# Kernel optimization log

Measured on AMD Instinct MI355X. Metric: run time of the kernel, lower is better.

The kernel has to match this reference:

```python
import jax, jax.numpy as jnp
import numpy as np

BN_EPS = 1e-5
NORM_EPS = 1e-12  # F.normalize default eps


def reference(x, conv_w, bn_gamma, bn_beta):
    # 1x1 conv dimension reduction: [B,2048,H,W] -> [B,256,H,W]
    z = jnp.einsum('bchw,dc->bdhw', x, conv_w)
    # BatchNorm2d (training-mode batch statistics) + ReLU
    mu = z.mean(axis=(0, 2, 3), keepdims=True)
    var = z.var(axis=(0, 2, 3), keepdims=True)
    z = (z - mu) / jnp.sqrt(var + BN_EPS)
    z = z * bn_gamma.reshape(1, -1, 1, 1) + bn_beta.reshape(1, -1, 1, 1)
    z = jax.nn.relu(z)

    B, d, h, w = z.shape
    M = h * w
    xm = z.reshape(B, d, M)
    # Covpool: y = x I_hat x^T with I_hat = (I - 11^T/M)/M == centered 2nd moment
    xc = xm - xm.mean(axis=-1, keepdims=True)
    cov = jnp.einsum('bdm,bem->bde', xc, xc) / M  # [B,d,d]

    # Eigen decomposition (cov is symmetric PSD; SVD of PSD == eigh)
    s, U = jnp.linalg.eigh(cov)  # s: [B,d], U: [B,d,d]
    eps = jnp.finfo(cov.dtype).eps
    s = jnp.maximum(s, eps)

    # ExponentialInverse: U exp(-S) U^T
    inv_x = jnp.einsum('bid,bd,bjd->bij', U, jnp.exp(-s), U)
    # Power (matrix sqrt): U S^{1/2} U^T
    out = jnp.einsum('bid,bd,bjd->bij', U, jnp.sqrt(s), U)

    # attention = out @ inv_x^T  (inv_x is symmetric, transpose kept for fidelity)
    att = jnp.einsum('bij,bkj->bik', out, inv_x)
    flat = att.reshape(B, -1)
    nrm = jnp.maximum(jnp.linalg.norm(flat, axis=1, keepdims=True), NORM_EPS)
    normalized = (flat / nrm).reshape(att.shape)
    att = out * (att / normalized)

    y = att + out
    iu = jnp.triu_indices(d)
    return y[:, iu[0], iu[1]]  # [B, d*(d+1)/2]


def setup_inputs() -> dict:
    key = jax.random.key(0)
    k1, k2 = jax.random.split(key)
    x = jax.random.normal(k1, (32, 2048, 28, 28), dtype=jnp.float32)
    # kaiming-normal fan_out scaling for 1x1 conv: std = sqrt(2/fan_out)=sqrt(2/256)
    conv_w = jax.random.normal(k2, (256, 2048), dtype=jnp.float32) * np.sqrt(2.0 / 256.0)
    bn_gamma = jnp.ones((256,), dtype=jnp.float32)
    bn_beta = jnp.zeros((256,), dtype=jnp.float32)
    return {'x': x, 'conv_w': conv_w, 'bn_gamma': bn_gamma, 'bn_beta': bn_beta}
```

## Files before the change

### kernel.cpp

```cpp
#include <hip/hip_runtime.h>


typedef unsigned short u16;
typedef __attribute__((ext_vector_type(8))) short bf16x8;
typedef __attribute__((ext_vector_type(4))) float f32x4;

__device__ __forceinline__ u16 f2bf(float f) {
  unsigned u = __builtin_bit_cast(unsigned, f);
  u += 0x7FFFu + ((u >> 16) & 1u);
  return (u16)(u >> 16);
}
__device__ __forceinline__ float bf2f(u16 h) {
  unsigned u = ((unsigned)h) << 16;
  return __builtin_bit_cast(float, u);
}

__device__ __forceinline__
void mm_core(const u16* __restrict__ Ah, const u16* __restrict__ Al,
             const u16* __restrict__ Bh, const u16* __restrict__ Bl,
             long boff, int row0, int col0,
             u16 (*lds)[128][8][8], f32x4 acc[4][4])
{
  const int tid = threadIdx.x;
  const int wave = tid >> 6, lane = tid & 63;
  const int wm = wave >> 1, wn = wave & 1;
  const int mL = lane & 15, q = lane >> 4;
  const u16* baseA[2] = {Ah + boff, Al + boff};
  const u16* baseB[2] = {Bh + boff, Bl + boff};

  for (int k0 = 0; k0 < 256; k0 += 64) {
    __syncthreads();
#pragma unroll
    for (int it = 0; it < 16; ++it) {
      const int t = it >> 2;
      const int r = ((it & 3) << 8) + tid;
      const int m = r >> 3, c = r & 7;
      const u16* src = (t < 2 ? baseA[t] : baseB[t - 2])
                     + (long)((t < 2 ? row0 : col0) + m) * 256 + k0 + c * 8;
      const uint4 v = *reinterpret_cast<const uint4*>(src);
      *reinterpret_cast<uint4*>(&lds[t][m][c ^ (m & 7)][0]) = v;
    }
    __syncthreads();
#pragma unroll
    for (int kk = 0; kk < 2; ++kk) {
      bf16x8 ah[4], al[4], bh[4], bl[4];
#pragma unroll
      for (int i = 0; i < 4; ++i) {
        const int ma = wm * 64 + i * 16 + mL;
        const int ca = (kk * 4 + q) ^ (ma & 7);
        ah[i] = *reinterpret_cast<const bf16x8*>(&lds[0][ma][ca][0]);
        al[i] = *reinterpret_cast<const bf16x8*>(&lds[1][ma][ca][0]);
        const int nb = wn * 64 + i * 16 + mL;
        const int cb = (kk * 4 + q) ^ (nb & 7);
        bh[i] = *reinterpret_cast<const bf16x8*>(&lds[2][nb][cb][0]);
        bl[i] = *reinterpret_cast<const bf16x8*>(&lds[3][nb][cb][0]);
      }
#pragma unroll
      for (int i = 0; i < 4; ++i)
#pragma unroll
        for (int j = 0; j < 4; ++j) {
          acc[i][j] = __builtin_amdgcn_mfma_f32_16x16x32_bf16(ah[i], bh[j], acc[i][j], 0, 0, 0);
          acc[i][j] = __builtin_amdgcn_mfma_f32_16x16x32_bf16(ah[i], bl[j], acc[i][j], 0, 0, 0);
          acc[i][j] = __builtin_amdgcn_mfma_f32_16x16x32_bf16(al[i], bh[j], acc[i][j], 0, 0, 0);
        }
    }
  }
}

template<int MB>
__global__ __launch_bounds__(256)
void fuse_k(const u16* __restrict__ A0, const u16* __restrict__ B0, u16* __restrict__ C0,
            float al0, float b10, float dg0, const float* __restrict__ cf0,
            const u16* __restrict__ A1, const u16* __restrict__ B1, u16* __restrict__ C1,
            u16* __restrict__ D1, float al1, float b11, float dg1,
            float hc1, float hc2, float hc3, const float* __restrict__ cf1, long LO)
{
  __shared__ u16 lds[4][128][8][8];
  int z = blockIdx.z;
  const bool hB = (z >= 32);
  const u16 *Ah, *Bh; u16 *C, *D = nullptr;
  float al, b1, dg; const float* cf;
  if (!hB) { Ah = A0; Bh = B0; C = C0; al = al0; b1 = b10; dg = dg0; cf = cf0; }
  else { z -= 32; Ah = A1; Bh = B1; C = C1; D = D1; al = al1; b1 = b11; dg = dg1; cf = cf1; }
  const long boff = (long)z * 65536;
  const int row0 = blockIdx.y * 128, col0 = blockIdx.x * 128;
  const int wave = threadIdx.x >> 6, lane = threadIdx.x & 63;
  const int wm = wave >> 1, wn = wave & 1;
  const int mL = lane & 15, q = lane >> 4;

  f32x4 acc[4][4];
#pragma unroll
  for (int i = 0; i < 4; ++i)
#pragma unroll
    for (int j = 0; j < 4; ++j) acc[i][j] = {0.f, 0.f, 0.f, 0.f};

  mm_core(Ah, Ah + LO, Bh, Bh + LO, boff, row0, col0, lds, acc);

#pragma unroll
  for (int i = 0; i < 4; ++i) {
    const int rbase = row0 + wm * 64 + i * 16 + q * 4;
#pragma unroll
    for (int j = 0; j < 4; ++j) {
      const int cc = col0 + wn * 64 + j * 16 + mL;
#pragma unroll
      for (int rg = 0; rg < 4; ++rg) {
        const int rr = rbase + rg;
        const long o = boff + (long)rr * 256 + cc;
        const float vr = acc[i][j][rg];
        if (MB == 1 && hB) {
          u16 h = f2bf(vr);
          C[o] = h; C[o + LO] = f2bf(vr - bf2f(h));
          float hv = fmaf(vr, hc1, cf[o] * hc2);
          if (rr == cc) hv += hc3;
          h = f2bf(hv);
          D[o] = h; D[o + LO] = f2bf(hv - bf2f(h));
        } else {
          float v = al * vr;
          if (cf) v = fmaf(b1, cf[o], v);
          if (rr == cc) v += dg;
          const u16 h = f2bf(v);
          C[o] = h; C[o + LO] = f2bf(v - bf2f(h));
        }
      }
    }
  }
}

__global__ __launch_bounds__(256)
void gemm2_pair_k(const u16* __restrict__ A0, const u16* __restrict__ B0, u16* __restrict__ C0,
                  const u16* __restrict__ A1, const u16* __restrict__ B1, u16* __restrict__ C1,
                  long LO)
{
  __shared__ u16 lds[4][128][8][8];
  int z = blockIdx.z;
  const u16 *Ah, *Bh; u16* Chp;
  if (z < 32) { Ah = A0; Bh = B0; Chp = C0; }
  else { z -= 32; Ah = A1; Bh = B1; Chp = C1; }
  const long boff = (long)z * 65536;
  const int row0 = blockIdx.y * 128, col0 = blockIdx.x * 128;
  const int wave = threadIdx.x >> 6, lane = threadIdx.x & 63;
  const int wm = wave >> 1, wn = wave & 1;
  const int mL = lane & 15, q = lane >> 4;

  f32x4 acc[4][4];
#pragma unroll
  for (int i = 0; i < 4; ++i)
#pragma unroll
    for (int j = 0; j < 4; ++j) acc[i][j] = {0.f, 0.f, 0.f, 0.f};

  mm_core(Ah, Ah + LO, Bh, Bh + LO, boff, row0, col0, lds, acc);

#pragma unroll
  for (int i = 0; i < 4; ++i) {
    const int rbase = row0 + wm * 64 + i * 16 + q * 4;
#pragma unroll
    for (int j = 0; j < 4; ++j) {
      const int cc = col0 + wn * 64 + j * 16 + mL;
#pragma unroll
      for (int rg = 0; rg < 4; ++rg) {
        const long o = boff + (long)(rbase + rg) * 256 + cc;
        const float v = acc[i][j][rg];
        const u16 h = f2bf(v);
        Chp[o] = h; Chp[o + LO] = f2bf(v - bf2f(h));
      }
    }
  }
}

template<int MODE>
__global__ __launch_bounds__(256)
void gemmN64_k(const u16* __restrict__ Ah, const u16* __restrict__ Al,
               const u16* __restrict__ Bh, const u16* __restrict__ Bl,
               u16* __restrict__ Ch, u16* __restrict__ Cl,
               const float* __restrict__ cf, float alpha, float b1, float diag,
               float* __restrict__ attn2)
{
  __shared__ u16 ldsA[2][128][8][8];
  __shared__ u16 ldsB[2][64][8][8];
  const long boff = (long)blockIdx.z * 65536;
  const int row0 = blockIdx.y * 128, col0 = blockIdx.x * 64;
  const int tid = threadIdx.x;
  const int wave = tid >> 6, lane = tid & 63;
  const int wm = wave >> 1, wn = wave & 1;
  const int mL = lane & 15, q = lane >> 4;
  const u16* baseA[2] = {Ah + boff, Al + boff};
  const u16* baseB[2] = {Bh + boff, Bl + boff};

  f32x4 acc[4][2];
#pragma unroll
  for (int i = 0; i < 4; ++i)
#pragma unroll
    for (int j = 0; j < 2; ++j) acc[i][j] = {0.f, 0.f, 0.f, 0.f};

  for (int k0 = 0; k0 < 256; k0 += 64) {
    __syncthreads();
#pragma unroll
    for (int it = 0; it < 8; ++it) {
      const int t = it >> 2;
      const int r = ((it & 3) << 8) + tid;
      const int m = r >> 3, c = r & 7;
      const uint4 v = *reinterpret_cast<const uint4*>(
          baseA[t] + (long)(row0 + m) * 256 + k0 + c * 8);
      *reinterpret_cast<uint4*>(&ldsA[t][m][c ^ (m & 7)][0]) = v;
    }
#pragma unroll
    for (int it = 0; it < 4; ++it) {
      const int t = it >> 1;
      const int r = ((it & 1) << 8) + tid;
      const int m = r >> 3, c = r & 7;
      const uint4 v = *reinterpret_cast<const uint4*>(
          baseB[t] + (long)(col0 + m) * 256 + k0 + c * 8);
      *reinterpret_cast<uint4*>(&ldsB[t][m][c ^ (m & 7)][0]) = v;
    }
    __syncthreads();
#pragma unroll
    for (int kk = 0; kk < 2; ++kk) {
      bf16x8 ah[4], alo[4], bh[2], bl[2];
#pragma unroll
      for (int i = 0; i < 4; ++i) {
        const int ma = wm * 64 + i * 16 + mL;
        const int ca = (kk * 4 + q) ^ (ma & 7);
        ah[i]  = *reinterpret_cast<const bf16x8*>(&ldsA[0][ma][ca][0]);
        alo[i] = *reinterpret_cast<const bf16x8*>(&ldsA[1][ma][ca][0]);
      }
#pragma unroll
      for (int j = 0; j < 2; ++j) {
        const int nb = wn * 32 + j * 16 + mL;
        const int cb = (kk * 4 + q) ^ (nb & 7);
        bh[j] = *reinterpret_cast<const bf16x8*>(&ldsB[0][nb][cb][0]);
        bl[j] = *reinterpret_cast<const bf16x8*>(&ldsB[1][nb][cb][0]);
      }
#pragma unroll
      for (int i = 0; i < 4; ++i)
#pragma unroll
        for (int j = 0; j < 2; ++j) {
          acc[i][j] = __builtin_amdgcn_mfma_f32_16x16x32_bf16(ah[i],  bh[j], acc[i][j], 0, 0, 0);
          acc[i][j] = __builtin_amdgcn_mfma_f32_16x16x32_bf16(ah[i],  bl[j], acc[i][j], 0, 0, 0);
          acc[i][j] = __builtin_amdgcn_mfma_f32_16x16x32_bf16(alo[i], bh[j], acc[i][j], 0, 0, 0);
        }
    }
  }

  if (MODE == 2) {
    float ssum = 0.f;
#pragma unroll
    for (int i = 0; i < 4; ++i)
#pragma unroll
      for (int j = 0; j < 2; ++j)
#pragma unroll
        for (int rg = 0; rg < 4; ++rg) ssum = fmaf(acc[i][j][rg], acc[i][j][rg], ssum);
#pragma unroll
    for (int o = 32; o > 0; o >>= 1) ssum += __shfl_down(ssum, o);
    __syncthreads();
    float* red = (float*)&ldsA[0][0][0][0];
    if (lane == 0) red[wave] = ssum;
    __syncthreads();
    if (tid == 0)
      atomicAdd(attn2 + blockIdx.z, red[0] + red[1] + red[2] + red[3]);
    return;
  }

#pragma unroll
  for (int i = 0; i < 4; ++i) {
    const int rbase = row0 + wm * 64 + i * 16 + q * 4;
#pragma unroll
    for (int j = 0; j < 2; ++j) {
      const int cc = col0 + wn * 32 + j * 16 + mL;
#pragma unroll
      for (int rg = 0; rg < 4; ++rg) {
        const int rr = rbase + rg;
        const long o = boff + (long)rr * 256 + cc;
        float v = alpha * acc[i][j][rg];
        if (cf) v = fmaf(b1, cf[o], v);
        if (rr == cc) v += diag;
        const u16 h = f2bf(v);
        Ch[o] = h; Cl[o] = f2bf(v - bf2f(h));
      }
    }
  }
}

__global__ __launch_bounds__(256)
void conv_k(const u16* __restrict__ wb, const float* __restrict__ x,
            float* __restrict__ z)
{
  __shared__ u16 ldsA[128][8][8];
  __shared__ u16 ldsB[128][8][8];
  const int tid = threadIdx.x;
  const int b = blockIdx.z;
  const int n0 = blockIdx.x * 128;
  const int m0 = blockIdx.y * 128;
  const int wave = tid >> 6, lane = tid & 63;
  const int wm = wave >> 1, wn = wave & 1;
  const int mL = lane & 15, q = lane >> 4;
  const float* xb = x + (long)b * 2048 * 784;

  f32x4 acc[4][4];
#pragma unroll
  for (int i = 0; i < 4; ++i)
#pragma unroll
    for (int j = 0; j < 4; ++j) acc[i][j] = {0.f, 0.f, 0.f, 0.f};

  for (int k0 = 0; k0 < 2048; k0 += 64) {
    __syncthreads();
#pragma unroll
    for (int it = 0; it < 4; ++it) {
      const int g = it * 256 + tid;
      const int m = g >> 3, c = g & 7;
      const uint4 v = *reinterpret_cast<const uint4*>(
          wb + (long)(m0 + m) * 2048 + k0 + c * 8);
      *reinterpret_cast<uint4*>(&ldsA[m][c ^ (m & 7)][0]) = v;
    }
    {
      const int kg = tid >> 5, nc = tid & 31;
      const int nbase = nc * 4;
      const int gn = n0 + nbase;
#pragma unroll
      for (int half = 0; half < 2; ++half) {
        const int kbase = kg * 4 + half * 32;
        float vv[4][4];
#pragma unroll
        for (int jk = 0; jk < 4; ++jk) {
          const int gk = k0 + kbase + jk;
          float4 f = make_float4(0.f, 0.f, 0.f, 0.f);
          if (gn < 784) f = *reinterpret_cast<const float4*>(xb + (long)gk * 784 + gn);
          vv[jk][0] = f.x; vv[jk][1] = f.y; vv[jk][2] = f.z; vv[jk][3] = f.w;
        }
        const int c = kbase >> 3, ko = kbase & 7;
#pragma unroll
        for (int jn = 0; jn < 4; ++jn) {
          const int n = nbase + jn;
          ushort4 u;
          u.x = f2bf(vv[0][jn]); u.y = f2bf(vv[1][jn]);
          u.z = f2bf(vv[2][jn]); u.w = f2bf(vv[3][jn]);
          *reinterpret_cast<ushort4*>(&ldsB[n][c ^ (n & 7)][ko]) = u;
        }
      }
    }
    __syncthreads();
#pragma unroll
    for (int kk = 0; kk < 2; ++kk) {
      bf16x8 af[4], bfv[4];
#pragma unroll
      for (int i = 0; i < 4; ++i) {
        const int ma = wm * 64 + i * 16 + mL;
        af[i] = *reinterpret_cast<const bf16x8*>(&ldsA[ma][(kk * 4 + q) ^ (ma & 7)][0]);
        const int nb = wn * 64 + i * 16 + mL;
        bfv[i] = *reinterpret_cast<const bf16x8*>(&ldsB[nb][(kk * 4 + q) ^ (nb & 7)][0]);
      }
#pragma unroll
      for (int i = 0; i < 4; ++i)
#pragma unroll
        for (int j = 0; j < 4; ++j)
          acc[i][j] = __builtin_amdgcn_mfma_f32_16x16x32_bf16(af[i], bfv[j], acc[i][j], 0, 0, 0);
    }
  }
#pragma unroll
  for (int i = 0; i < 4; ++i) {
    const int rbase = m0 + wm * 64 + i * 16 + q * 4;
#pragma unroll
    for (int j = 0; j < 4; ++j) {
      const int cc = n0 + wn * 64 + j * 16 + mL;
      if (cc >= 784) continue;
#pragma unroll
      for (int rg = 0; rg < 4; ++rg)
        z[((long)b * 256 + rbase + rg) * 784 + cc] = acc[i][j][rg];
    }
  }
}

__global__ __launch_bounds__(256)
void gram_k(const u16* __restrict__ zb, const float* __restrict__ rs,
            float* __restrict__ cov, u16* __restrict__ C2h, u16* __restrict__ C2l)
{
  __shared__ u16 lds[2][128][8][8];
  const int tid = threadIdx.x;
  const int b = blockIdx.z;
  const int col0 = blockIdx.x * 128, row0 = blockIdx.y * 128;
  const int wave = tid >> 6, lane = tid & 63;
  const int wm = wave >> 1, wn = wave & 1;
  const int mL = lane & 15, q = lane >> 4;
  const u16* zbb = zb + (long)b * 256 * 832;

  f32x4 acc[4][4];
#pragma unroll
  for (int i = 0; i < 4; ++i)
#pragma unroll
    for (int j = 0; j < 4; ++j) acc[i][j] = {0.f, 0.f, 0.f, 0.f};

  for (int k0 = 0; k0 < 832; k0 += 64) {
    __syncthreads();
#pragma unroll
    for (int it = 0; it < 8; ++it) {
      const int t = it >> 2;
      const int r = ((it & 3) << 8) + tid;
      const int m = r >> 3, c = r & 7;
      const int grow = (t == 0 ? row0 : col0) + m;
      const uint4 v = *reinterpret_cast<const uint4*>(zbb + (long)grow * 832 + k0 + c * 8);
      *reinterpret_cast<uint4*>(&lds[t][m][c ^ (m & 7)][0]) = v;
    }
    __syncthreads();
#pragma unroll
    for (int kk = 0; kk < 2; ++kk) {
      bf16x8 af[4], bfv[4];
#pragma unroll
      for (int i = 0; i < 4; ++i) {
        const int ma = wm * 64 + i * 16 + mL;
        af[i] = *reinterpret_cast<const bf16x8*>(&lds[0][ma][(kk * 4 + q) ^ (ma & 7)][0]);
        const int nb = wn * 64 + i * 16 + mL;
        bfv[i] = *reinterpret_cast<const bf16x8*>(&lds[1][nb][(kk * 4 + q) ^ (nb & 7)][0]);
      }
#pragma unroll
      for (int i = 0; i < 4; ++i)
#pragma unroll
        for (int j = 0; j < 4; ++j)
          acc[i][j] = __builtin_amdgcn_mfma_f32_16x16x32_bf16(af[i], bfv[j], acc[i][j], 0, 0, 0);
    }
  }
  const float inv_m = 1.f / 784.f;
#pragma unroll
  for (int i = 0; i < 4; ++i) {
    const int rr0 = row0 + wm * 64 + i * 16 + q * 4;
#pragma unroll
    for (int j = 0; j < 4; ++j) {
      const int cc = col0 + wn * 64 + j * 16 + mL;
      const float mu_c = rs[b * 256 + cc] * inv_m;
#pragma unroll
      for (int rg = 0; rg < 4; ++rg) {
        const int rr = rr0 + rg;
        const float mu_r = rs[b * 256 + rr] * inv_m;
        const long o = ((long)b * 256 + rr) * 256 + cc;
        const float cv = fmaf(acc[i][j][rg], inv_m, -mu_r * mu_c);
        cov[o] = cv;
        const u16 h = f2bf(cv);
        C2h[o] = h; C2l[o] = f2bf(cv - bf2f(h));
      }
    }
  }
}

__global__ __launch_bounds__(256)
void bn_stats_k(const float* __restrict__ z, float* __restrict__ ps,
                float* __restrict__ pq)
{
  const int d = blockIdx.x, sl = blockIdx.y, t = threadIdx.x;
  const int lane = t & 63, wid = t >> 6;
  __shared__ float ws[4], wq[4];
  float s = 0.f, qq = 0.f;
  for (int b = sl * 4; b < sl * 4 + 4; ++b) {
    const float* p = z + ((long)b * 256 + d) * 784;
    for (int m = t; m < 784; m += 256) {
      const float v = p[m];
      s += v; qq = fmaf(v, v, qq);
    }
  }
#pragma unroll
  for (int o = 32; o > 0; o >>= 1) { s += __shfl_down(s, o); qq += __shfl_down(qq, o); }
  if (lane == 0) { ws[wid] = s; wq[wid] = qq; }
  __syncthreads();
  if (t == 0) {
    ps[d * 8 + sl] = ws[0] + ws[1] + ws[2] + ws[3];
    pq[d * 8 + sl] = wq[0] + wq[1] + wq[2] + wq[3];
  }
}

__global__ __launch_bounds__(256)
void bn_apply_k(const float* __restrict__ z, const float* __restrict__ gamma,
                const float* __restrict__ beta, const float* __restrict__ ps,
                const float* __restrict__ pq, u16* __restrict__ zb,
                float* __restrict__ rs)
{
  const int d = blockIdx.x, b = blockIdx.y, t = threadIdx.x;
  const int lane = t & 63, wid = t >> 6;
  __shared__ float bc[2], ws[4];
  if (t == 0) {
    float sum = 0.f, sq = 0.f;
#pragma unroll
    for (int s8 = 0; s8 < 8; ++s8) { sum += ps[d * 8 + s8]; sq += pq[d * 8 + s8]; }
    const float inv_n = 1.f / 25088.f;
    const float mean = sum * inv_n;
    const float var = sq * inv_n - mean * mean;
    const float sc = gamma[d] * rsqrtf(var + 1e-5f);
    bc[0] = sc; bc[1] = fmaf(-mean, sc, beta[d]);
  }
  __syncthreads();
  const float sc = bc[0], sh = bc[1];
  const float* p = z + ((long)b * 256 + d) * 784;
  u16* qp = zb + ((long)b * 256 + d) * 832;
  float rsum = 0.f;
  for (int m = t; m < 832; m += 256) {
    const float v = (m < 784) ? fmaxf(fmaf(p[m], sc, sh), 0.f) : 0.f;
    qp[m] = f2bf(v);
    rsum += v;
  }
#pragma unroll
  for (int o = 32; o > 0; o >>= 1) rsum += __shfl_down(rsum, o);
  if (lane == 0) ws[wid] = rsum;
  __syncthreads();
  if (t == 0) rs[b * 256 + d] = ws[0] + ws[1] + ws[2] + ws[3];
}

__global__ __launch_bounds__(1024)
void power_k(const float* __restrict__ cov, float* __restrict__ s,
             float* __restrict__ attn2)
{
  const int b = blockIdx.x, tid = threadIdx.x;
  const int i = tid & 255, g = tid >> 8;
  const float* A = cov + (long)b * 65536;
  __shared__ float v[256];
  __shared__ float part[4][256];
  __shared__ float red[4];
  if (g == 0) v[i] = 1.f;
  __syncthreads();
  float lam = 1.f;
  for (int it = 0; it < 10; ++it) {
    float u = 0.f;
    const int jb = g * 64;
#pragma unroll 8
    for (int j = jb; j < jb + 64; ++j) u = fmaf(A[(long)j * 256 + i], v[j], u);
    part[g][i] = u;
    __syncthreads();
    if (g == 0) {
      u = part[0][i] + part[1][i] + part[2][i] + part[3][i];
      float ss = u * u;
#pragma unroll
      for (int o = 32; o > 0; o >>= 1) ss += __shfl_down(ss, o);
      if ((i & 63) == 0) red[i >> 6] = ss;
    }
    __syncthreads();
    lam = sqrtf(red[0] + red[1] + red[2] + red[3]);
    if (g == 0) v[i] = u / lam;
    __syncthreads();
  }
  if (tid == 0) { s[b] = 1.8f / lam; attn2[b] = 0.f; }
}

__global__ __launch_bounds__(256)
void init_k(const float* __restrict__ cov, const float* __restrict__ s,
            u16* __restrict__ Yh, u16* __restrict__ Yl,
            u16* __restrict__ Th, u16* __restrict__ Tl)
{
  const int b = blockIdx.y, i = blockIdx.x, j = threadIdx.x;
  const long o = ((long)b * 256 + i) * 256 + j;
  const float a = cov[o] * s[b];
  u16 h = f2bf(a);
  Yh[o] = h; Yl[o] = f2bf(a - bf2f(h));
  float tv = -0.5f * a;
  if (i == j) tv += 1.5f;
  h = f2bf(tv);
  Th[o] = h; Tl[o] = f2bf(tv - bf2f(h));
}

__global__ __launch_bounds__(256)
void out_k(const u16* __restrict__ Yh, const u16* __restrict__ Yl,
           const float* __restrict__ s, const float* __restrict__ attn2,
           float* __restrict__ out)
{
  const int i = blockIdx.x, b = blockIdx.y, j = threadIdx.x;
  if (j < i) return;
  const float inv = rsqrtf(s[b]);
  const float nrm = fmaxf(sqrtf(fmaxf(attn2[b], 0.f)) * inv, 1e-12f);
  const float scv = inv * (1.f + nrm);
  const long o = ((long)b * 256 + i) * 256 + j;
  const long off = (long)b * 32896 + (long)i * 256 - (long)i * (i - 1) / 2 + (j - i);
  out[off] = (bf2f(Yh[o]) + bf2f(Yl[o])) * scv;
}

__global__ __launch_bounds__(256)
void cast_w_k(const float* __restrict__ w, u16* __restrict__ wb)
{
  const int idx = blockIdx.x * 256 + threadIdx.x;
  wb[idx] = f2bf(w[idx]);
}

extern "C" void kernel_launch(void* const* d_in, const int* in_sizes, int n_in,
                              void* d_out, int out_size, void* d_ws, size_t ws_size,
                              hipStream_t stream)
{
  const float* x     = (const float*)d_in[0];
  const float* w     = (const float*)d_in[1];
  const float* gamma = (const float*)d_in[2];
  const float* beta  = (const float*)d_in[3];
  float* out = (float*)d_out;

  const long PS = 4194304;
  const long LO = 2097152;
  u16* S[9];
  for (int k = 0; k < 9; ++k) S[k] = (u16*)d_ws + (long)k * PS;
  char* base = (char*)d_ws;
  float* z   = (float*)(base + 75497472);
  u16*   zb  = (u16*)(base + 101187584);
  float* cov = (float*)(base + 114819072);
  u16*   wbuf = (u16*)(base + 114819072);
  float* st  = (float*)(base + 123207680);
  float* sv = st, *attn2 = st + 32, *rs = st + 64;
  float* ps = st + 64 + 8192, *pq = ps + 2048;
  u16 *C2 = S[5], *V = S[6], *Ha = S[7], *Hb = S[8];

  const dim3 blk(256);
  const dim3 gP(2, 2, 64);
  const dim3 gT(4, 2, 32);
  const dim3 gE(256, 32);

  cast_w_k<<<dim3(2048), blk, 0, stream>>>(w, wbuf);
  conv_k<<<dim3(7, 2, 32), blk, 0, stream>>>(wbuf, x, z);
  bn_stats_k<<<dim3(256, 8), blk, 0, stream>>>(z, ps, pq);
  bn_apply_k<<<dim3(256, 32), blk, 0, stream>>>(z, gamma, beta, ps, pq, zb, rs);
  gram_k<<<dim3(2, 2, 32), blk, 0, stream>>>(zb, rs, cov, C2, C2 + LO);
  power_k<<<dim3(32), dim3(1024), 0, stream>>>(cov, sv, attn2);
  init_k<<<gE, blk, 0, stream>>>(cov, sv, S[0], S[0] + LO, S[1], S[1] + LO);

  fuse_k<1><<<gP, blk, 0, stream>>>(
      S[0], S[1], S[2], 1.f, 0.f, 0.f, (const float*)nullptr,
      C2, C2, V, Ha, 1.f, 0.f, 0.f,
      1.f / 40320.f, -1.f / 5040.f, 1.f / 720.f, cov, LO);

  int iY = 2, iZ = 1, fa = 0, fb = 3, fc = 4;
  for (int it = 1; it <= 7; ++it) {
    const int iT = fa;
    if (it == 1)
      fuse_k<0><<<gP, blk, 0, stream>>>(
          S[iZ], S[iY], S[iT], -0.5f, 0.f, 1.5f, (const float*)nullptr,
          V, Ha, Hb, (u16*)nullptr, 1.f, -1.f / 120.f, 1.f / 24.f,
          0.f, 0.f, 0.f, cov, LO);
    else if (it == 2)
      fuse_k<0><<<gP, blk, 0, stream>>>(
          S[iZ], S[iY], S[iT], -0.5f, 0.f, 1.5f, (const float*)nullptr,
          V, Hb, Ha, (u16*)nullptr, 1.f, -1.f / 6.f, 0.5f,
          0.f, 0.f, 0.f, cov, LO);
    else if (it == 3)
      fuse_k<0><<<gP, blk, 0, stream>>>(
          S[iZ], S[iY], S[iT], -0.5f, 0.f, 1.5f, (const float*)nullptr,
          V, Ha, Hb, (u16*)nullptr, 1.f, -1.f, 1.f,
          0.f, 0.f, 0.f, cov, LO);
    else
      gemmN64_k<0><<<gT, blk, 0, stream>>>(
          S[iZ], S[iZ] + LO, S[iY], S[iY] + LO, S[iT], S[iT] + LO,
          (const float*)nullptr, -0.5f, 0.f, 1.5f, (float*)nullptr);
    if (it < 7) {
      gemm2_pair_k<<<gP, blk, 0, stream>>>(S[iY], S[iT], S[fb],
                                           S[iT], S[iZ], S[fc], LO);
      const int nY = fb, nZ = fc;
      fa = iY; fb = iZ; fc = iT;
      iY = nY; iZ = nZ;
    } else {
      gemmN64_k<0><<<gT, blk, 0, stream>>>(
          S[iY], S[iY] + LO, S[iT], S[iT] + LO, S[fb], S[fb] + LO,
          (const float*)nullptr, 1.f, 0.f, 0.f, (float*)nullptr);
      iY = fb;
    }
  }

  gemmN64_k<2><<<gT, blk, 0, stream>>>(
      S[iY], S[iY] + LO, Hb, Hb + LO, (u16*)nullptr, (u16*)nullptr,
      (const float*)nullptr, 1.f, 0.f, 0.f, attn2);
  out_k<<<gE, blk, 0, stream>>>(S[iY], S[iY] + LO, sv, attn2, out);
}
```

Before: 739.0 us.

## Split conv GEMM along K with smaller M tiles and sum partials in BN

The 1x1 conv GEMM is split into two K halves with 64-row M tiles, quadrupling the block count to fill the GPU better. The two partial outputs go to separate buffers and are summed inside the BN statistics and apply kernels. The cost is that x is re-read by more M tiles, and an extra fp32 z buffer is written and read twice. The x load path is also reorganized into 8 consecutive k rows per thread with two LDS stores.

```diff
diff --git a/kernel.cpp b/kernel.cpp
--- a/kernel.cpp
+++ b/kernel.cpp
@@ -282,89 +282,96 @@
 
 __global__ __launch_bounds__(256)
 void conv_k(const u16* __restrict__ wb, const float* __restrict__ x,
-            float* __restrict__ z)
-{
-  __shared__ u16 ldsA[128][8][8];
+            float* __restrict__ z0, float* __restrict__ z1)
+{
+  __shared__ u16 ldsA[64][8][8];
   __shared__ u16 ldsB[128][8][8];
   const int tid = threadIdx.x;
   const int b = blockIdx.z;
   const int n0 = blockIdx.x * 128;
-  const int m0 = blockIdx.y * 128;
+  const int m0 = (blockIdx.y & 3) * 64;
+  const int ks = blockIdx.y >> 2;
+  const int kb0 = ks * 1024;
   const int wave = tid >> 6, lane = tid & 63;
   const int wm = wave >> 1, wn = wave & 1;
   const int mL = lane & 15, q = lane >> 4;
   const float* xb = x + (long)b * 2048 * 784;
-
-  f32x4 acc[4][4];
-#pragma unroll
-  for (int i = 0; i < 4; ++i)
+  float* zp = (ks == 0 ? z0 : z1);
+
+  f32x4 acc[2][4];
+#pragma unroll
+  for (int i = 0; i < 2; ++i)
 #pragma unroll
     for (int j = 0; j < 4; ++j) acc[i][j] = {0.f, 0.f, 0.f, 0.f};
 
-  for (int k0 = 0; k0 < 2048; k0 += 64) {
-    __syncthreads();
-#pragma unroll
-    for (int it = 0; it < 4; ++it) {
+  const int kc = tid >> 5, nc = tid & 31;
+  const int nbase = nc * 4;
+  const int gn = n0 + nbase;
+
+  for (int k0 = 0; k0 < 1024; k0 += 64) {
+    const int kg = kb0 + k0;
+    __syncthreads();
+#pragma unroll
+    for (int it = 0; it < 2; ++it) {
       const int g = it * 256 + tid;
       const int m = g >> 3, c = g & 7;
       const uint4 v = *reinterpret_cast<const uint4*>(
-          wb + (long)(m0 + m) * 2048 + k0 + c * 8);
+          wb + (long)(m0 + m) * 2048 + kg + c * 8);
       *reinterpret_cast<uint4*>(&ldsA[m][c ^ (m & 7)][0]) = v;
     }
     {
-      const int kg = tid >> 5, nc = tid & 31;
-      const int nbase = nc * 4;
-      const int gn = n0 + nbase;
-#pragma unroll
-      for (int half = 0; half < 2; ++half) {
-        const int kbase = kg * 4 + half * 32;
-        float vv[4][4];
-#pragma unroll
-        for (int jk = 0; jk < 4; ++jk) {
-          const int gk = k0 + kbase + jk;
-          float4 f = make_float4(0.f, 0.f, 0.f, 0.f);
-          if (gn < 784) f = *reinterpret_cast<const float4*>(xb + (long)gk * 784 + gn);
-          vv[jk][0] = f.x; vv[jk][1] = f.y; vv[jk][2] = f.z; vv[jk][3] = f.w;
-        }
-        const int c = kbase >> 3, ko = kbase & 7;
-#pragma unroll
-        for (int jn = 0; jn < 4; ++jn) {
-          const int n = nbase + jn;
-          ushort4 u;
-          u.x = f2bf(vv[0][jn]); u.y = f2bf(vv[1][jn]);
-          u.z = f2bf(vv[2][jn]); u.w = f2bf(vv[3][jn]);
-          *reinterpret_cast<ushort4*>(&ldsB[n][c ^ (n & 7)][ko]) = u;
-        }
+      float vv[8][4];
+#pragma unroll
+      for (int jk = 0; jk < 8; ++jk) {
+        float4 f = make_float4(0.f, 0.f, 0.f, 0.f);
+        if (gn < 784)
+          f = *reinterpret_cast<const float4*>(xb + (long)(kg + kc * 8 + jk) * 784 + gn);
+        vv[jk][0] = f.x; vv[jk][1] = f.y; vv[jk][2] = f.z; vv[jk][3] = f.w;
+      }
+#pragma unroll
+      for (int jn = 0; jn < 4; ++jn) {
+        const int n = nbase + jn;
+        const int ch = kc ^ (n & 7);
+        ushort4 ua, ub;
+        ua.x = f2bf(vv[0][jn]); ua.y = f2bf(vv[1][jn]);
+        ua.z = f2bf(vv[2][jn]); ua.w = f2bf(vv[3][jn]);
+        ub.x = f2bf(vv[4][jn]); ub.y = f2bf(vv[5][jn]);
+        ub.z = f2bf(vv[6][jn]); ub.w = f2bf(vv[7][jn]);
+        *reinterpret_cast<ushort4*>(&ldsB[n][ch][0]) = ua;
+        *reinterpret_cast<ushort4*>(&ldsB[n][ch][4]) = ub;
       }
     }
     __syncthreads();
 #pragma unroll
     for (int kk = 0; kk < 2; ++kk) {
-      bf16x8 af[4], bfv[4];
-#pragma unroll
-      for (int i = 0; i < 4; ++i) {
-        const int ma = wm * 64 + i * 16 + mL;
+      bf16x8 af[2], bfv[4];
+#pragma unroll
+      for (int i = 0; i < 2; ++i) {
+        const int ma = wm * 32 + i * 16 + mL;
         af[i] = *reinterpret_cast<const bf16x8*>(&ldsA[ma][(kk * 4 + q) ^ (ma & 7)][0]);
-        const int nb = wn * 64 + i * 16 + mL;
-        bfv[i] = *reinterpret_cast<const bf16x8*>(&ldsB[nb][(kk * 4 + q) ^ (nb & 7)][0]);
-      }
-#pragma unroll
-      for (int i = 0; i < 4; ++i)
+      }
+#pragma unroll
+      for (int j = 0; j < 4; ++j) {
+        const int nb = wn * 64 + j * 16 + mL;
+        bfv[j] = *reinterpret_cast<const bf16x8*>(&ldsB[nb][(kk * 4 + q) ^ (nb & 7)][0]);
+      }
+#pragma unroll
+      for (int i = 0; i < 2; ++i)
 #pragma unroll
         for (int j = 0; j < 4; ++j)
           acc[i][j] = __builtin_amdgcn_mfma_f32_16x16x32_bf16(af[i], bfv[j], acc[i][j], 0, 0, 0);
     }
   }
 #pragma unroll
-  for (int i = 0; i < 4; ++i) {
-    const int rbase = m0 + wm * 64 + i * 16 + q * 4;
+  for (int i = 0; i < 2; ++i) {
+    const int rbase = m0 + wm * 32 + i * 16 + q * 4;
 #pragma unroll
     for (int j = 0; j < 4; ++j) {
       const int cc = n0 + wn * 64 + j * 16 + mL;
       if (cc >= 784) continue;
 #pragma unroll
       for (int rg = 0; rg < 4; ++rg)
-        z[((long)b * 256 + rbase + rg) * 784 + cc] = acc[i][j][rg];
+        zp[((long)b * 256 + rbase + rg) * 784 + cc] = acc[i][j][rg];
     }
   }
 }
@@ -440,17 +447,17 @@
 }
 
 __global__ __launch_bounds__(256)
-void bn_stats_k(const float* __restrict__ z, float* __restrict__ ps,
-                float* __restrict__ pq)
+void bn_stats_k(const float* __restrict__ z0, const float* __restrict__ z1,
+                float* __restrict__ ps, float* __restrict__ pq)
 {
   const int d = blockIdx.x, sl = blockIdx.y, t = threadIdx.x;
   const int lane = t & 63, wid = t >> 6;
   __shared__ float ws[4], wq[4];
   float s = 0.f, qq = 0.f;
   for (int b = sl * 4; b < sl * 4 + 4; ++b) {
-    const float* p = z + ((long)b * 256 + d) * 784;
+    const long off = ((long)b * 256 + d) * 784;
     for (int m = t; m < 784; m += 256) {
-      const float v = p[m];
+      const float v = z0[off + m] + z1[off + m];
       s += v; qq = fmaf(v, v, qq);
     }
   }
@@ -465,10 +472,10 @@
 }
 
 __global__ __launch_bounds__(256)
-void bn_apply_k(const float* __restrict__ z, const float* __restrict__ gamma,
-                const float* __restrict__ beta, const float* __restrict__ ps,
-                const float* __restrict__ pq, u16* __restrict__ zb,
-                float* __restrict__ rs)
+void bn_apply_k(const float* __restrict__ z0, const float* __restrict__ z1,
+                const float* __restrict__ gamma, const float* __restrict__ beta,
+                const float* __restrict__ ps, const float* __restrict__ pq,
+                u16* __restrict__ zb, float* __restrict__ rs)
 {
   const int d = blockIdx.x, b = blockIdx.y, t = threadIdx.x;
   const int lane = t & 63, wid = t >> 6;
@@ -485,11 +492,12 @@
   }
   __syncthreads();
   const float sc = bc[0], sh = bc[1];
-  const float* p = z + ((long)b * 256 + d) * 784;
+  const long off = ((long)b * 256 + d) * 784;
   u16* qp = zb + ((long)b * 256 + d) * 832;
   float rsum = 0.f;
   for (int m = t; m < 832; m += 256) {
-    const float v = (m < 784) ? fmaxf(fmaf(p[m], sc, sh), 0.f) : 0.f;
+    const float v = (m < 784)
+        ? fmaxf(fmaf(z0[off + m] + z1[off + m], sc, sh), 0.f) : 0.f;
     qp[m] = f2bf(v);
     rsum += v;
   }
@@ -588,11 +596,12 @@
   u16* S[9];
   for (int k = 0; k < 9; ++k) S[k] = (u16*)d_ws + (long)k * PS;
   char* base = (char*)d_ws;
-  float* z   = (float*)(base + 75497472);
-  u16*   zb  = (u16*)(base + 101187584);
-  float* cov = (float*)(base + 114819072);
-  u16*   wbuf = (u16*)(base + 114819072);
-  float* st  = (float*)(base + 123207680);
+  float* z0  = (float*)(base + 75497472);
+  float* z1  = (float*)(base + 101187584);
+  u16*   zb  = (u16*)(base + 126877696);
+  float* cov = (float*)(base + 140509184);
+  u16*   wbuf = (u16*)(base + 140509184);
+  float* st  = (float*)(base + 148897792);
   float* sv = st, *attn2 = st + 32, *rs = st + 64;
   float* ps = st + 64 + 8192, *pq = ps + 2048;
   u16 *C2 = S[5], *V = S[6], *Ha = S[7], *Hb = S[8];
@@ -603,9 +612,9 @@
   const dim3 gE(256, 32);
 
   cast_w_k<<<dim3(2048), blk, 0, stream>>>(w, wbuf);
-  conv_k<<<dim3(7, 2, 32), blk, 0, stream>>>(wbuf, x, z);
-  bn_stats_k<<<dim3(256, 8), blk, 0, stream>>>(z, ps, pq);
-  bn_apply_k<<<dim3(256, 32), blk, 0, stream>>>(z, gamma, beta, ps, pq, zb, rs);
+  conv_k<<<dim3(7, 8, 32), blk, 0, stream>>>(wbuf, x, z0, z1);
+  bn_stats_k<<<dim3(256, 8), blk, 0, stream>>>(z0, z1, ps, pq);
+  bn_apply_k<<<dim3(256, 32), blk, 0, stream>>>(z0, z1, gamma, beta, ps, pq, zb, rs);
   gram_k<<<dim3(2, 2, 32), blk, 0, stream>>>(zb, rs, cov, C2, C2 + LO);
   power_k<<<dim3(32), dim3(1024), 0, stream>>>(cov, sv, attn2);
   init_k<<<gE, blk, 0, stream>>>(cov, sv, S[0], S[0] + LO, S[1], S[1] + LO);
```

Measured after the change: 742.7 us. No clear change (+0.5%).
